# Kernel optimization log

Measured on AMD Instinct MI355X. Metric: run time of the kernel, lower is better.

Reference implementation:

```python
import jax, jax.numpy as jnp
import numpy as np

B, N, D, H = 2, 2048, 768, 12
HD = D // H


def setup_inputs() -> dict:
    key = jax.random.key(0)
    ks = jax.random.split(key, 8)
    x = jax.random.normal(ks[0], (B, N, D), dtype=jnp.float32)
    dist = jax.random.randint(ks[1], (B, N, N), 0, 32, dtype=jnp.int32)
    mask = jax.random.bernoulli(ks[2], 0.1, (B, N))  # True = masked key
    # parameters (torch Linear stored pre-transposed: y = x @ W + b)
    s = 1.0 / np.sqrt(D)
    qkv_w = jax.random.uniform(ks[3], (D, 3 * D), jnp.float32, -s, s)
    qkv_b = jax.random.uniform(ks[4], (3 * D,), jnp.float32, -s, s)
    out_w = jax.random.uniform(ks[5], (D, D), jnp.float32, -s, s)
    out_b = jax.random.uniform(ks[6], (D,), jnp.float32, -s, s)
    bias_table = jax.random.normal(ks[7], (32, H), dtype=jnp.float32)
    return {"x": x, "dist": dist, "mask": mask, "qkv_w": qkv_w,
            "qkv_b": qkv_b, "out_w": out_w, "out_b": out_b,
            "bias_table": bias_table}


def reference(x, dist, mask, qkv_w, qkv_b, out_w, out_b, bias_table):
    scale = HD ** -0.5
    qkv = x @ qkv_w + qkv_b                      # [B,N,3D]
    q, k, v = jnp.split(qkv, 3, axis=-1)
    sh = lambda t: t.reshape(B, N, H, HD).transpose(0, 2, 1, 3)  # [B,H,N,HD]
    q, k, v = sh(q), sh(k), sh(v)
    a = jnp.einsum('bhnd,bhmd->bhnm', q, k) * scale  # [B,H,N,N]
    # relative-position bias: gather [B,N,N,H] -> [B,H,N,N]
    a = a + bias_table[jnp.clip(dist, 0, 31)].transpose(0, 3, 1, 2)
    a = jnp.where(mask[:, None, None, :], -jnp.inf, a)
    a = jax.nn.softmax(a.astype(jnp.float32), axis=-1)  # dropout: eval mode (p ignored)
    o = jnp.einsum('bhnm,bhmd->bhnd', a, v)            # [B,H,N,HD]
    o = o.transpose(0, 2, 1, 3).reshape(B, N, D)
    return o @ out_w + out_b
```

## Files before the change

kernel.cpp:

```cpp
#include <hip/hip_runtime.h>
#include <hip/hip_bf16.h>

typedef unsigned short u16;
typedef __attribute__((ext_vector_type(8))) short bf16x8;
typedef __attribute__((ext_vector_type(4))) float f32x4;

#define MFMA_BF16(a,b,c) __builtin_amdgcn_mfma_f32_16x16x32_bf16((a),(b),(c),0,0,0)
#define LOG2E 1.4426950408889634f

__device__ __forceinline__ u16 f2b(float f) {
    __hip_bfloat16 h = __float2bfloat16(f);
    u16 u; __builtin_memcpy(&u, &h, 2); return u;
}
__device__ __forceinline__ f32x4 zero4() { f32x4 z = {0.f,0.f,0.f,0.f}; return z; }

__device__ __forceinline__ void gl_lds16(const u16* g, u16* l) {
    __builtin_amdgcn_global_load_lds(
        (const __attribute__((address_space(1))) unsigned int*)g,
        (__attribute__((address_space(3))) unsigned int*)l,
        16, 0, 0);
}

__global__ __launch_bounds__(256) void convX(const float* __restrict__ in, u16* __restrict__ out) {
    size_t i = ((size_t)blockIdx.x * 256 + threadIdx.x) * 8;
    float4 a = *(const float4*)(in + i);
    float4 b = *(const float4*)(in + i + 4);
    union { u16 s[8]; uint4 v; } u;
    u.s[0]=f2b(a.x); u.s[1]=f2b(a.y); u.s[2]=f2b(a.z); u.s[3]=f2b(a.w);
    u.s[4]=f2b(b.x); u.s[5]=f2b(b.y); u.s[6]=f2b(b.z); u.s[7]=f2b(b.w);
    *(uint4*)(out + i) = u.v;
}

__global__ __launch_bounds__(256) void packDist(const int* __restrict__ din, unsigned char* __restrict__ dout) {
    size_t i = ((size_t)blockIdx.x * 256 + threadIdx.x) * 4;
    int4 v = *(const int4*)(din + i);
    uchar4 o;
    o.x = (unsigned char)min(max(v.x, 0), 31);
    o.y = (unsigned char)min(max(v.y, 0), 31);
    o.z = (unsigned char)min(max(v.z, 0), 31);
    o.w = (unsigned char)min(max(v.w, 0), 31);
    *(uchar4*)(dout + i) = o;
}

__global__ __launch_bounds__(256) void convTW(const float* __restrict__ in, u16* __restrict__ out, int C) {
    __shared__ __align__(16) u16 T[64][68];
    int c0 = blockIdx.x * 64, k0 = blockIdx.y * 64;
    int tid = threadIdx.x;
#pragma unroll
    for (int i = 0; i < 4; ++i) {
        int id = tid + i * 256;
        int row = id >> 4, ch = id & 15;
        float4 v = *(const float4*)(in + (size_t)(k0 + row) * C + c0 + ch * 4);
        T[row][ch*4+0] = f2b(v.x); T[row][ch*4+1] = f2b(v.y);
        T[row][ch*4+2] = f2b(v.z); T[row][ch*4+3] = f2b(v.w);
    }
    __syncthreads();
#pragma unroll
    for (int i = 0; i < 2; ++i) {
        int id = tid + i * 256;
        int c = id >> 3, ch = id & 7;
        union { u16 s[8]; uint4 v; } u;
#pragma unroll
        for (int j = 0; j < 8; ++j) u.s[j] = T[ch*8+j][c];
        *(uint4*)(out + (size_t)(c0 + c) * 768 + k0 + ch * 8) = u.v;
    }
}

__global__ void detectMaskBits(const unsigned* __restrict__ m, unsigned long long* __restrict__ mbits) {
    __shared__ int sB, sH, sF;
    if (threadIdx.x == 0) { sB = 0; sH = 0; sF = 0; }
    __syncthreads();
    int lb = 0, lh = 0, lf = 0;
#pragma unroll
    for (int i = 0; i < 4; ++i) {
        unsigned v = m[threadIdx.x + i * 256];
        if (v == 0x3f800000u) { lf = 1; }
        else if (v > 1u) {
            unsigned b0 = v & 0xffu, b1 = (v >> 8) & 0xffu, b2 = (v >> 16) & 0xffu, b3 = v >> 24;
            bool bytesOK = (b0 <= 1u) && (b1 <= 1u) && (b2 <= 1u) && (b3 <= 1u);
            unsigned h0 = v & 0xffffu, h1 = v >> 16;
            bool halfOK = (h0 == 0u || h0 == 0x3f80u) && (h1 == 0u || h1 == 0x3f80u);
            if (bytesOK) lb = 1; else if (halfOK) lh = 1;
        }
    }
    if (lb) atomicOr(&sB, 1);
    if (lh) atomicOr(&sH, 1);
    if (lf) atomicOr(&sF, 1);
    __syncthreads();
    int mode = sH ? 3 : (sB ? 1 : (sF ? 2 : 0));
    const unsigned char* m8 = (const unsigned char*)m;
    const u16* mh = (const u16*)m;
    const float* mf = (const float*)m;
    const int* mi = (const int*)m;
    for (int it = 0; it < 16; ++it) {
        int e = it * 256 + threadIdx.x;
        int pred;
        if (mode == 0)      pred = (mi[e] != 0);
        else if (mode == 1) pred = (m8[e] != 0);
        else if (mode == 2) pred = (mf[e] != 0.0f);
        else                pred = (mh[e] != 0);
        unsigned long long bal = __ballot(pred);
        if ((threadIdx.x & 63) == 0) mbits[it * 4 + (threadIdx.x >> 6)] = bal;
    }
}

template<int MODE>
__global__ __launch_bounds__(256)
void gemmBT(const u16* __restrict__ A, const u16* __restrict__ Bt,
            const float* __restrict__ bias,
            u16* __restrict__ qO, u16* __restrict__ kO, u16* __restrict__ vO,
            float* __restrict__ fO) {
    __shared__ __align__(16) u16 As[128][40];
    __shared__ __align__(16) u16 Bs[128][40];
    const int K = 768;
    const int tid = threadIdx.x;
    const int lane = tid & 63, w = tid >> 6;
    const int wm = w >> 1, wn = w & 1;
    const int l15 = lane & 15, q = lane >> 4;
    const int m0 = blockIdx.y * 128, n0 = blockIdx.x * 128;
    const int rowS = tid >> 1, cS = (tid & 1) * 2;
    const u16* Ag = A + (size_t)(m0 + rowS) * K;
    const u16* Bg = Bt + (size_t)(n0 + rowS) * K;
    uint4 pa0, pa1, pb0, pb1;
    { const uint4* sa = (const uint4*)Ag; pa0 = sa[cS]; pa1 = sa[cS+1];
      const uint4* sb = (const uint4*)Bg; pb0 = sb[cS]; pb1 = sb[cS+1]; }
    f32x4 acc[4][4];
#pragma unroll
    for (int i=0;i<4;++i)
#pragma unroll
        for (int j=0;j<4;++j) acc[i][j] = zero4();

    for (int kt = 0; kt < 24; ++kt) {
        __syncthreads();
        *(uint4*)&As[rowS][cS*8]   = pa0; *(uint4*)&As[rowS][cS*8+8] = pa1;
        *(uint4*)&Bs[rowS][cS*8]   = pb0; *(uint4*)&Bs[rowS][cS*8+8] = pb1;
        __syncthreads();
        if (kt < 23) {
            const uint4* sa = (const uint4*)(Ag + (kt+1)*32);
            pa0 = sa[cS]; pa1 = sa[cS+1];
            const uint4* sb = (const uint4*)(Bg + (kt+1)*32);
            pb0 = sb[cS]; pb1 = sb[cS+1];
        }
        bf16x8 af[4], bfr[4];
#pragma unroll
        for (int mt=0; mt<4; ++mt) af[mt]  = *(const bf16x8*)&As[wm*64+mt*16+l15][q*8];
#pragma unroll
        for (int nt=0; nt<4; ++nt) bfr[nt] = *(const bf16x8*)&Bs[wn*64+nt*16+l15][q*8];
#pragma unroll
        for (int mt=0; mt<4; ++mt)
#pragma unroll
            for (int nt=0; nt<4; ++nt)
                acc[mt][nt] = MFMA_BF16(af[mt], bfr[nt], acc[mt][nt]);
    }

#pragma unroll
    for (int mt=0; mt<4; ++mt) {
#pragma unroll
        for (int nt=0; nt<4; ++nt) {
            int n = n0 + wn*64 + nt*16 + l15;
            float bv = bias[n];
            if (MODE == 0) {
                int which = n / 768;
                int rem = n - which*768;
                int hh = rem >> 6, hd = rem & 63;
                int mBase = m0 + wm*64 + mt*16 + q*4;
                int b = mBase >> 11, tok0 = mBase & 2047;
                if (which == 2) {
                    union { u16 s4[4]; unsigned long long u; } pv;
#pragma unroll
                    for (int r=0; r<4; ++r) pv.s4[r] = f2b(acc[mt][nt][r] + bv);
                    *(unsigned long long*)(vO + ((size_t)(b*12 + hh)*64 + hd)*2048 + tok0) = pv.u;
                } else {
#pragma unroll
                    for (int r=0; r<4; ++r) {
                        float v = acc[mt][nt][r] + bv;
                        size_t di = (((size_t)(b*12 + hh))*2048 + tok0 + r)*64 + hd;
                        if (which == 0) qO[di] = f2b(v * (0.125f * LOG2E));
                        else            kO[di] = f2b(v);
                    }
                }
            } else {
#pragma unroll
                for (int r=0; r<4; ++r) {
                    int m = m0 + wm*64 + mt*16 + q*4 + r;
                    fO[(size_t)m*768 + n] = acc[mt][nt][r] + bv;
                }
            }
        }
    }
}

__global__ __launch_bounds__(256)
void flashAttn(const u16* __restrict__ Qb, const u16* __restrict__ Kb,
               const u16* __restrict__ Vt, const unsigned char* __restrict__ dist8,
               const unsigned long long* __restrict__ mbits,
               const float* __restrict__ btg, u16* __restrict__ attnout) {
    __shared__ float bt[32];
    __shared__ __align__(16) u16 KT[2][4096];
    __shared__ __align__(16) u16 VT[2][4096];
    __shared__ __align__(16) u16 Os[4][16][72];
    const int tid = threadIdx.x;
    const int lane = tid & 63, w = tid >> 6;
    const int l15 = lane & 15, q = lane >> 4;
    const int wg = blockIdx.x + 32 * (blockIdx.y + 12 * blockIdx.z);
    const int xcd = wg & 7, slot = wg >> 3;
    const int g = ((slot >> 5) << 3) + xcd;
    const int i0 = (slot & 31) * 64;
    const int b = g / 12, h = g - b * 12;
    const int bh = g;
    const float NEG_INF = -__builtin_inff();
    if (tid < 32) bt[tid] = btg[tid*12 + h] * LOG2E;

    const int iRow = i0 + w*16 + l15;
    const u16* Qp = Qb + ((size_t)bh*2048 + iRow)*64;
    bf16x8 qB0 = *(const bf16x8*)(Qp + q*8);
    bf16x8 qB1 = *(const bf16x8*)(Qp + 32 + q*8);
    const unsigned char* dp = dist8 + ((size_t)(b*2048 + iRow))*2048 + q*4;
    const unsigned long long* mbp = mbits + b*32;
    const int srcL0 = ((2*q)   & 3)*16 + l15;
    const int srcL1 = ((2*q+1) & 3)*16 + l15;
    union { unsigned u4[4]; bf16x8 v; } one_;
    { unsigned oc = (l15 == 0) ? 0x3F803F80u : 0u;
      one_.u4[0]=oc; one_.u4[1]=oc; one_.u4[2]=oc; one_.u4[3]=oc; }

    const int stRow = w*16 + (lane >> 3);
    const int stCol = (((lane & 7) ^ (lane >> 3)) << 4);
    const char* kgB = (const char*)Kb + (size_t)bh*2048*128;
    const char* vgB = (const char*)Vt + (size_t)bh*64*4096;
    const int swz = (l15 & 7) << 4;
    const int f0 = (q*16)      ^ swz;
    const int f1 = (q*16 + 64) ^ swz;
    const int rB = l15 * 128;

    {
        u16* kd = &KT[0][0] + w*1024;
        u16* vd = &VT[0][0] + w*1024;
#pragma unroll
        for (int c = 0; c < 2; ++c) {
            int row = stRow + c*8;
            gl_lds16((const u16*)(kgB + (size_t)row*128 + stCol),  kd + c*512);
            gl_lds16((const u16*)(vgB + (size_t)row*4096 + stCol), vd + c*512);
        }
    }
    __syncthreads();

    f32x4 o0 = zero4(), o1 = zero4(), o2 = zero4(), o3 = zero4(), o4 = zero4();
    float mI = NEG_INF;
    int cur = 0;

    for (int jt = 0; jt < 32; ++jt) {
        const int j0 = jt * 64;
        if (jt < 31) {
            const int j0n = j0 + 64;
            u16* kd = &KT[cur^1][0] + w*1024;
            u16* vd = &VT[cur^1][0] + w*1024;
#pragma unroll
            for (int c = 0; c < 2; ++c) {
                int row = stRow + c*8;
                gl_lds16((const u16*)(kgB + (size_t)(j0n + row)*128 + stCol), kd + c*512);
                gl_lds16((const u16*)(vgB + (size_t)row*4096 + (size_t)j0n*2 + stCol), vd + c*512);
            }
        }
        unsigned dv4[4];
#pragma unroll
        for (int mt = 0; mt < 4; ++mt) dv4[mt] = *(const unsigned*)(dp + j0 + mt*16);
        unsigned long long mb = mbp[jt];

        const char* kt = (const char*)&KT[cur][0];
        f32x4 s0 = zero4(), s1 = zero4(), s2 = zero4(), s3 = zero4();
        {
            bf16x8 k00 = *(const bf16x8*)(kt + rB          + f0);
            bf16x8 k01 = *(const bf16x8*)(kt + rB          + f1);
            bf16x8 k10 = *(const bf16x8*)(kt + rB + 2048   + f0);
            bf16x8 k11 = *(const bf16x8*)(kt + rB + 2048   + f1);
            bf16x8 k20 = *(const bf16x8*)(kt + rB + 4096   + f0);
            bf16x8 k21 = *(const bf16x8*)(kt + rB + 4096   + f1);
            bf16x8 k30 = *(const bf16x8*)(kt + rB + 6144   + f0);
            bf16x8 k31 = *(const bf16x8*)(kt + rB + 6144   + f1);
            __builtin_amdgcn_s_setprio(1);
            s0 = MFMA_BF16(k00, qB0, s0); s0 = MFMA_BF16(k01, qB1, s0);
            s1 = MFMA_BF16(k10, qB0, s1); s1 = MFMA_BF16(k11, qB1, s1);
            s2 = MFMA_BF16(k20, qB0, s2); s2 = MFMA_BF16(k21, qB1, s2);
            s3 = MFMA_BF16(k30, qB0, s3); s3 = MFMA_BF16(k31, qB1, s3);
            __builtin_amdgcn_s_setprio(0);
        }

        unsigned long long ms = mb >> (q*4);
        unsigned mlo = (unsigned)ms, mhi = (unsigned)(ms >> 32);
        float sv[4][4];
#pragma unroll
        for (int mt = 0; mt < 4; ++mt) {
            const f32x4 sm = mt==0 ? s0 : (mt==1 ? s1 : (mt==2 ? s2 : s3));
            const unsigned d4 = dv4[mt];
#pragma unroll
            for (int r = 0; r < 4; ++r) {
                int dd = (d4 >> (r*8)) & 255;
                float x = sm[r] + bt[dd];
                unsigned bit = (mt < 2) ? ((mlo >> (mt*16 + r)) & 1u)
                                        : ((mhi >> ((mt-2)*16 + r)) & 1u);
                sv[mt][r] = bit ? NEG_INF : x;
            }
        }

        float t0 = fmaxf(fmaxf(sv[0][0], sv[0][1]), fmaxf(sv[0][2], sv[0][3]));
        float t1 = fmaxf(fmaxf(sv[1][0], sv[1][1]), fmaxf(sv[1][2], sv[1][3]));
        float t2 = fmaxf(fmaxf(sv[2][0], sv[2][1]), fmaxf(sv[2][2], sv[2][3]));
        float t3 = fmaxf(fmaxf(sv[3][0], sv[3][1]), fmaxf(sv[3][2], sv[3][3]));
        float rm = fmaxf(fmaxf(t0, t1), fmaxf(t2, t3));
        rm = fmaxf(rm, __shfl_xor(rm, 16, 64));
        rm = fmaxf(rm, __shfl_xor(rm, 32, 64));
        if (!__all(rm <= mI)) {
            float mn = fmaxf(mI, rm);
            float al = exp2f(mI - mn);
            mI = mn;
#pragma unroll
            for (int r = 0; r < 4; ++r) { o0[r] *= al; o1[r] *= al; o2[r] *= al; o3[r] *= al; }
            o4[0] *= al;
        }
        float p[4][4];
#pragma unroll
        for (int mt = 0; mt < 4; ++mt)
#pragma unroll
            for (int r = 0; r < 4; ++r) p[mt][r] = exp2f(sv[mt][r] - mI);

        unsigned pk[4][2];
#pragma unroll
        for (int mt = 0; mt < 4; ++mt) {
            pk[mt][0] = (unsigned)f2b(p[mt][0]) | ((unsigned)f2b(p[mt][1]) << 16);
            pk[mt][1] = (unsigned)f2b(p[mt][2]) | ((unsigned)f2b(p[mt][3]) << 16);
        }
        const char* vt = (const char*)&VT[cur][0];
        __builtin_amdgcn_s_setprio(1);
#pragma unroll
        for (int ks = 0; ks < 2; ++ks) {
            union { unsigned d[4]; bf16x8 v; } pb;
#pragma unroll
            for (int s = 0; s < 4; ++s) {
                int sl = (s >> 1) ? srcL1 : srcL0;
                int u0 = __shfl((int)pk[2*ks    ][s & 1], sl, 64);
                int u1 = __shfl((int)pk[2*ks + 1][s & 1], sl, 64);
                pb.d[s] = (q >> 1) ? (unsigned)u1 : (unsigned)u0;
            }
            const int fk = ks ? f1 : f0;
            bf16x8 v0 = *(const bf16x8*)(vt + rB          + fk);
            bf16x8 v1 = *(const bf16x8*)(vt + rB + 2048   + fk);
            bf16x8 v2 = *(const bf16x8*)(vt + rB + 4096   + fk);
            bf16x8 v3 = *(const bf16x8*)(vt + rB + 6144   + fk);
            o0 = MFMA_BF16(v0, pb.v, o0);
            o1 = MFMA_BF16(v1, pb.v, o1);
            o2 = MFMA_BF16(v2, pb.v, o2);
            o3 = MFMA_BF16(v3, pb.v, o3);
            o4 = MFMA_BF16(one_.v, pb.v, o4);
        }
        __builtin_amdgcn_s_setprio(0);

        __syncthreads();
        cur ^= 1;
    }

    float lsum = __shfl(o4[0], l15, 64);
    float inv = 1.0f / lsum;
#pragma unroll
    for (int r = 0; r < 4; ++r) {
        Os[w][l15][ 0 + q*4 + r] = f2b(o0[r] * inv);
        Os[w][l15][16 + q*4 + r] = f2b(o1[r] * inv);
        Os[w][l15][32 + q*4 + r] = f2b(o2[r] * inv);
        Os[w][l15][48 + q*4 + r] = f2b(o3[r] * inv);
    }
    __syncthreads();
    int rr = lane >> 2, cc = lane & 3;
    uint4 a0 = *(const uint4*)&Os[w][rr][cc*16];
    uint4 a1 = *(const uint4*)&Os[w][rr][cc*16 + 8];
    size_t orow = ((size_t)b*2048 + i0 + w*16 + rr)*768 + h*64 + cc*16;
    *(uint4*)(attnout + orow)     = a0;
    *(uint4*)(attnout + orow + 8) = a1;
}

extern "C" void kernel_launch(void* const* d_in, const int* in_sizes, int n_in,
                              void* d_out, int out_size, void* d_ws, size_t ws_size,
                              hipStream_t stream) {
    (void)in_sizes; (void)n_in; (void)out_size; (void)ws_size;
    const float* x      = (const float*)d_in[0];
    const int*   dist   = (const int*)d_in[1];
    const int*   mask   = (const int*)d_in[2];
    const float* qkv_w  = (const float*)d_in[3];
    const float* qkv_b  = (const float*)d_in[4];
    const float* out_w  = (const float*)d_in[5];
    const float* out_b  = (const float*)d_in[6];
    const float* btab   = (const float*)d_in[7];
    float* out = (float*)d_out;

    char* ws = (char*)d_ws;
    size_t off = 0;
    auto alloc = [&](size_t bytes) { void* p = ws + off; off += (bytes + 255) & ~(size_t)255; return p; };
    u16* xb      = (u16*)alloc((size_t)4096*768*2);
    u16* wqkvT   = (u16*)alloc((size_t)2304*768*2);
    u16* woutT   = (u16*)alloc((size_t)768*768*2);
    u16* Qb      = (u16*)alloc((size_t)24*2048*64*2);
    u16* Kb      = (u16*)alloc((size_t)24*2048*64*2);
    u16* Vtp     = (u16*)alloc((size_t)24*2048*64*2);
    u16* attnout = (u16*)alloc((size_t)4096*768*2);
    unsigned char* dist8 = (unsigned char*)alloc((size_t)2*2048*2048);
    unsigned long long* mbits = (unsigned long long*)alloc(64*8);

    convX<<<1536, 256, 0, stream>>>(x, xb);
    packDist<<<8192, 256, 0, stream>>>(dist, dist8);
    convTW<<<dim3(36,12), 256, 0, stream>>>(qkv_w, wqkvT, 2304);
    convTW<<<dim3(12,12), 256, 0, stream>>>(out_w, woutT, 768);
    detectMaskBits<<<1, 256, 0, stream>>>((const unsigned*)mask, mbits);
    gemmBT<0><<<dim3(18,32), 256, 0, stream>>>(xb, wqkvT, qkv_b, Qb, Kb, Vtp, nullptr);
    flashAttn<<<dim3(32,12,2), 256, 0, stream>>>(Qb, Kb, Vtp, dist8, mbits, btab, attnout);
    gemmBT<1><<<dim3(6,32), 256, 0, stream>>>(attnout, woutT, out_b, nullptr, nullptr, nullptr, out);
}
```

Before: 259.5 us.

## Split attention over key halves with merge kernel; fold mask into dist codes

```diff
diff --git a/kernel.cpp b/kernel.cpp
--- a/kernel.cpp
+++ b/kernel.cpp
@@ -31,14 +31,19 @@
     *(uint4*)(out + i) = u.v;
 }
 
-__global__ __launch_bounds__(256) void packDist(const int* __restrict__ din, unsigned char* __restrict__ dout) {
+__global__ __launch_bounds__(256) void packDist(const int* __restrict__ din,
+                                                const unsigned long long* __restrict__ mbits,
+                                                unsigned char* __restrict__ dout) {
     size_t i = ((size_t)blockIdx.x * 256 + threadIdx.x) * 4;
     int4 v = *(const int4*)(din + i);
+    int b = (int)(i >> 22);
+    int j = (int)(i & 2047);
+    unsigned bits = (unsigned)((mbits[b*32 + (j >> 6)] >> (j & 63)) & 0xFull);
     uchar4 o;
-    o.x = (unsigned char)min(max(v.x, 0), 31);
-    o.y = (unsigned char)min(max(v.y, 0), 31);
-    o.z = (unsigned char)min(max(v.z, 0), 31);
-    o.w = (unsigned char)min(max(v.w, 0), 31);
+    o.x = (bits & 1u) ? 32 : (unsigned char)min(max(v.x, 0), 31);
+    o.y = (bits & 2u) ? 32 : (unsigned char)min(max(v.y, 0), 31);
+    o.z = (bits & 4u) ? 32 : (unsigned char)min(max(v.z, 0), 31);
+    o.w = (bits & 8u) ? 32 : (unsigned char)min(max(v.w, 0), 31);
     *(uchar4*)(dout + i) = o;
 }
 
@@ -193,12 +198,11 @@
 __global__ __launch_bounds__(256)
 void flashAttn(const u16* __restrict__ Qb, const u16* __restrict__ Kb,
                const u16* __restrict__ Vt, const unsigned char* __restrict__ dist8,
-               const unsigned long long* __restrict__ mbits,
-               const float* __restrict__ btg, u16* __restrict__ attnout) {
-    __shared__ float bt[32];
+               const float* __restrict__ btg,
+               float* __restrict__ Op, float* __restrict__ mlp) {
+    __shared__ float bt[33];
     __shared__ __align__(16) u16 KT[2][4096];
     __shared__ __align__(16) u16 VT[2][4096];
-    __shared__ __align__(16) u16 Os[4][16][72];
     const int tid = threadIdx.x;
     const int lane = tid & 63, w = tid >> 6;
     const int l15 = lane & 15, q = lane >> 4;
@@ -206,17 +210,17 @@
     const int xcd = wg & 7, slot = wg >> 3;
     const int g = ((slot >> 5) << 3) + xcd;
     const int i0 = (slot & 31) * 64;
-    const int b = g / 12, h = g - b * 12;
-    const int bh = g;
+    const int zz = g / 12, h = g - zz * 12;
+    const int b = zz >> 1, sIdx = zz & 1;
+    const int bh = b * 12 + h;
     const float NEG_INF = -__builtin_inff();
-    if (tid < 32) bt[tid] = btg[tid*12 + h] * LOG2E;
+    if (tid < 33) bt[tid] = (tid == 32) ? NEG_INF : btg[tid*12 + h] * LOG2E;
 
     const int iRow = i0 + w*16 + l15;
     const u16* Qp = Qb + ((size_t)bh*2048 + iRow)*64;
     bf16x8 qB0 = *(const bf16x8*)(Qp + q*8);
     bf16x8 qB1 = *(const bf16x8*)(Qp + 32 + q*8);
     const unsigned char* dp = dist8 + ((size_t)(b*2048 + iRow))*2048 + q*4;
-    const unsigned long long* mbp = mbits + b*32;
     const int srcL0 = ((2*q)   & 3)*16 + l15;
     const int srcL1 = ((2*q+1) & 3)*16 + l15;
     union { unsigned u4[4]; bf16x8 v; } one_;
@@ -232,14 +236,16 @@
     const int f1 = (q*16 + 64) ^ swz;
     const int rB = l15 * 128;
 
+    const int jtBeg = sIdx * 16, jtEnd = jtBeg + 16;
     {
+        const int j0p = jtBeg * 64;
         u16* kd = &KT[0][0] + w*1024;
         u16* vd = &VT[0][0] + w*1024;
 #pragma unroll
         for (int c = 0; c < 2; ++c) {
             int row = stRow + c*8;
-            gl_lds16((const u16*)(kgB + (size_t)row*128 + stCol),  kd + c*512);
-            gl_lds16((const u16*)(vgB + (size_t)row*4096 + stCol), vd + c*512);
+            gl_lds16((const u16*)(kgB + (size_t)(j0p + row)*128 + stCol),          kd + c*512);
+            gl_lds16((const u16*)(vgB + (size_t)row*4096 + (size_t)j0p*2 + stCol), vd + c*512);
         }
     }
     __syncthreads();
@@ -248,23 +254,22 @@
     float mI = NEG_INF;
     int cur = 0;
 
-    for (int jt = 0; jt < 32; ++jt) {
+    for (int jt = jtBeg; jt < jtEnd; ++jt) {
         const int j0 = jt * 64;
-        if (jt < 31) {
+        if (jt < jtEnd - 1) {
             const int j0n = j0 + 64;
             u16* kd = &KT[cur^1][0] + w*1024;
             u16* vd = &VT[cur^1][0] + w*1024;
 #pragma unroll
             for (int c = 0; c < 2; ++c) {
                 int row = stRow + c*8;
-                gl_lds16((const u16*)(kgB + (size_t)(j0n + row)*128 + stCol), kd + c*512);
+                gl_lds16((const u16*)(kgB + (size_t)(j0n + row)*128 + stCol),          kd + c*512);
                 gl_lds16((const u16*)(vgB + (size_t)row*4096 + (size_t)j0n*2 + stCol), vd + c*512);
             }
         }
         unsigned dv4[4];
 #pragma unroll
         for (int mt = 0; mt < 4; ++mt) dv4[mt] = *(const unsigned*)(dp + j0 + mt*16);
-        unsigned long long mb = mbp[jt];
 
         const char* kt = (const char*)&KT[cur][0];
         f32x4 s0 = zero4(), s1 = zero4(), s2 = zero4(), s3 = zero4();
@@ -285,8 +290,6 @@
             __builtin_amdgcn_s_setprio(0);
         }
 
-        unsigned long long ms = mb >> (q*4);
-        unsigned mlo = (unsigned)ms, mhi = (unsigned)(ms >> 32);
         float sv[4][4];
 #pragma unroll
         for (int mt = 0; mt < 4; ++mt) {
@@ -295,10 +298,7 @@
 #pragma unroll
             for (int r = 0; r < 4; ++r) {
                 int dd = (d4 >> (r*8)) & 255;
-                float x = sm[r] + bt[dd];
-                unsigned bit = (mt < 2) ? ((mlo >> (mt*16 + r)) & 1u)
-                                        : ((mhi >> ((mt-2)*16 + r)) & 1u);
-                sv[mt][r] = bit ? NEG_INF : x;
+                sv[mt][r] = sm[r] + bt[dd];
             }
         }
 
@@ -359,21 +359,51 @@
     }
 
     float lsum = __shfl(o4[0], l15, 64);
-    float inv = 1.0f / lsum;
-#pragma unroll
-    for (int r = 0; r < 4; ++r) {
-        Os[w][l15][ 0 + q*4 + r] = f2b(o0[r] * inv);
-        Os[w][l15][16 + q*4 + r] = f2b(o1[r] * inv);
-        Os[w][l15][32 + q*4 + r] = f2b(o2[r] * inv);
-        Os[w][l15][48 + q*4 + r] = f2b(o3[r] * inv);
-    }
-    __syncthreads();
-    int rr = lane >> 2, cc = lane & 3;
-    uint4 a0 = *(const uint4*)&Os[w][rr][cc*16];
-    uint4 a1 = *(const uint4*)&Os[w][rr][cc*16 + 8];
-    size_t orow = ((size_t)b*2048 + i0 + w*16 + rr)*768 + h*64 + cc*16;
-    *(uint4*)(attnout + orow)     = a0;
-    *(uint4*)(attnout + orow + 8) = a1;
+    if (q == 0) {
+        float2 v; v.x = mI; v.y = lsum;
+        *(float2*)(mlp + ((size_t)(sIdx*24 + bh)*2048 + i0 + w*16 + l15)*2) = v;
+    }
+    float* dst = Op + (((size_t)(sIdx*24 + bh)*2048 + i0 + w*16 + l15)*64 + q*4);
+    *(f32x4*)(dst)      = o0;
+    *(f32x4*)(dst + 16) = o1;
+    *(f32x4*)(dst + 32) = o2;
+    *(f32x4*)(dst + 48) = o3;
+}
+
+__global__ __launch_bounds__(256)
+void mergeO(const float* __restrict__ Op, const float* __restrict__ mlp,
+            u16* __restrict__ attnout) {
+    const int tid = threadIdx.x;
+    const int w = tid >> 6, lane = tid & 63;
+    const int rsub = lane >> 4, d0 = (lane & 15) * 4;
+    const int row = blockIdx.x * 16 + w * 4 + rsub;
+    const int bh = row >> 11, i = row & 2047;
+    const int b = bh / 12, h = bh - b * 12;
+    const float NEG_INF = -__builtin_inff();
+    float m[2], l[2];
+#pragma unroll
+    for (int s = 0; s < 2; ++s) {
+        float2 v = *(const float2*)(mlp + ((size_t)(s*24 + bh)*2048 + i)*2);
+        m[s] = v.x; l[s] = v.y;
+    }
+    float M = fmaxf(m[0], m[1]);
+    float a[2]; float L = 0.f;
+#pragma unroll
+    for (int s = 0; s < 2; ++s) {
+        a[s] = (m[s] == NEG_INF) ? 0.f : exp2f(m[s] - M);
+        L += l[s] * a[s];
+    }
+    float inv = 1.0f / L;
+    float4 o = {0.f, 0.f, 0.f, 0.f};
+#pragma unroll
+    for (int s = 0; s < 2; ++s) {
+        float4 v = *(const float4*)(Op + (((size_t)(s*24 + bh)*2048 + i)*64 + d0));
+        o.x += v.x * a[s]; o.y += v.y * a[s]; o.z += v.z * a[s]; o.w += v.w * a[s];
+    }
+    union { u16 s4[4]; unsigned long long u; } pk;
+    pk.s4[0] = f2b(o.x * inv); pk.s4[1] = f2b(o.y * inv);
+    pk.s4[2] = f2b(o.z * inv); pk.s4[3] = f2b(o.w * inv);
+    *(unsigned long long*)(attnout + ((size_t)(b*2048 + i))*768 + h*64 + d0) = pk.u;
 }
 
 extern "C" void kernel_launch(void* const* d_in, const int* in_sizes, int n_in,
@@ -400,15 +430,18 @@
     u16* Kb      = (u16*)alloc((size_t)24*2048*64*2);
     u16* Vtp     = (u16*)alloc((size_t)24*2048*64*2);
     u16* attnout = (u16*)alloc((size_t)4096*768*2);
+    float* Opart = (float*)alloc((size_t)2*24*2048*64*4);
+    float* mlPart= (float*)alloc((size_t)2*24*2048*2*4);
     unsigned char* dist8 = (unsigned char*)alloc((size_t)2*2048*2048);
     unsigned long long* mbits = (unsigned long long*)alloc(64*8);
 
     convX<<<1536, 256, 0, stream>>>(x, xb);
-    packDist<<<8192, 256, 0, stream>>>(dist, dist8);
+    detectMaskBits<<<1, 256, 0, stream>>>((const unsigned*)mask, mbits);
+    packDist<<<8192, 256, 0, stream>>>(dist, mbits, dist8);
     convTW<<<dim3(36,12), 256, 0, stream>>>(qkv_w, wqkvT, 2304);
     convTW<<<dim3(12,12), 256, 0, stream>>>(out_w, woutT, 768);
-    detectMaskBits<<<1, 256, 0, stream>>>((const unsigned*)mask, mbits);
     gemmBT<0><<<dim3(18,32), 256, 0, stream>>>(xb, wqkvT, qkv_b, Qb, Kb, Vtp, nullptr);
-    flashAttn<<<dim3(32,12,2), 256, 0, stream>>>(Qb, Kb, Vtp, dist8, mbits, btab, attnout);
+    flashAttn<<<dim3(32,12,4), 256, 0, stream>>>(Qb, Kb, Vtp, dist8, btab, Opart, mlPart);
+    mergeO<<<3072, 256, 0, stream>>>(Opart, mlPart, attnout);
     gemmBT<1><<<dim3(6,32), 256, 0, stream>>>(attnout, woutT, out_b, nullptr, nullptr, nullptr, out);
 }
```

Result: no change. 264.4 us (+1.9%).

## Fold key mask into packed dist sentinel and use 16x16x16 MFMA for PV

Applied to the files above, without the earlier changes.

```diff
diff --git a/kernel.cpp b/kernel.cpp
--- a/kernel.cpp
+++ b/kernel.cpp
@@ -3,10 +3,21 @@
 
 typedef unsigned short u16;
 typedef __attribute__((ext_vector_type(8))) short bf16x8;
+typedef __attribute__((ext_vector_type(4))) short bf16x4;
 typedef __attribute__((ext_vector_type(4))) float f32x4;
 
 #define MFMA_BF16(a,b,c) __builtin_amdgcn_mfma_f32_16x16x32_bf16((a),(b),(c),0,0,0)
 #define LOG2E 1.4426950408889634f
+
+#if __has_builtin(__builtin_amdgcn_mfma_f32_16x16x16bf16_1k)
+#define MFMA16(a,b,c) __builtin_amdgcn_mfma_f32_16x16x16bf16_1k((a),(b),(c),0,0,0)
+#define HAVE_MFMA16 1
+#elif __has_builtin(__builtin_amdgcn_mfma_f32_16x16x16_bf16)
+#define MFMA16(a,b,c) __builtin_amdgcn_mfma_f32_16x16x16_bf16((a),(b),(c),0,0,0)
+#define HAVE_MFMA16 1
+#else
+#define HAVE_MFMA16 0
+#endif
 
 __device__ __forceinline__ u16 f2b(float f) {
     __hip_bfloat16 h = __float2bfloat16(f);
@@ -31,14 +42,19 @@
     *(uint4*)(out + i) = u.v;
 }
 
-__global__ __launch_bounds__(256) void packDist(const int* __restrict__ din, unsigned char* __restrict__ dout) {
+__global__ __launch_bounds__(256) void packDist(const int* __restrict__ din,
+                                                const unsigned long long* __restrict__ mbits,
+                                                unsigned char* __restrict__ dout) {
     size_t i = ((size_t)blockIdx.x * 256 + threadIdx.x) * 4;
     int4 v = *(const int4*)(din + i);
+    int b = (int)(i >> 22);
+    int j = (int)(i & 2047);
+    unsigned bits = (unsigned)((mbits[b*32 + (j >> 6)] >> (j & 63)) & 0xFull);
     uchar4 o;
-    o.x = (unsigned char)min(max(v.x, 0), 31);
-    o.y = (unsigned char)min(max(v.y, 0), 31);
-    o.z = (unsigned char)min(max(v.z, 0), 31);
-    o.w = (unsigned char)min(max(v.w, 0), 31);
+    o.x = (bits & 1u) ? 32 : (unsigned char)min(max(v.x, 0), 31);
+    o.y = (bits & 2u) ? 32 : (unsigned char)min(max(v.y, 0), 31);
+    o.z = (bits & 4u) ? 32 : (unsigned char)min(max(v.z, 0), 31);
+    o.w = (bits & 8u) ? 32 : (unsigned char)min(max(v.w, 0), 31);
     *(uchar4*)(dout + i) = o;
 }
 
@@ -193,9 +209,8 @@
 __global__ __launch_bounds__(256)
 void flashAttn(const u16* __restrict__ Qb, const u16* __restrict__ Kb,
                const u16* __restrict__ Vt, const unsigned char* __restrict__ dist8,
-               const unsigned long long* __restrict__ mbits,
                const float* __restrict__ btg, u16* __restrict__ attnout) {
-    __shared__ float bt[32];
+    __shared__ float bt[33];
     __shared__ __align__(16) u16 KT[2][4096];
     __shared__ __align__(16) u16 VT[2][4096];
     __shared__ __align__(16) u16 Os[4][16][72];
@@ -209,19 +224,24 @@
     const int b = g / 12, h = g - b * 12;
     const int bh = g;
     const float NEG_INF = -__builtin_inff();
-    if (tid < 32) bt[tid] = btg[tid*12 + h] * LOG2E;
+    if (tid < 33) bt[tid] = (tid == 32) ? NEG_INF : btg[tid*12 + h] * LOG2E;
 
     const int iRow = i0 + w*16 + l15;
     const u16* Qp = Qb + ((size_t)bh*2048 + iRow)*64;
     bf16x8 qB0 = *(const bf16x8*)(Qp + q*8);
     bf16x8 qB1 = *(const bf16x8*)(Qp + 32 + q*8);
     const unsigned char* dp = dist8 + ((size_t)(b*2048 + iRow))*2048 + q*4;
-    const unsigned long long* mbp = mbits + b*32;
+#if !HAVE_MFMA16
     const int srcL0 = ((2*q)   & 3)*16 + l15;
     const int srcL1 = ((2*q+1) & 3)*16 + l15;
     union { unsigned u4[4]; bf16x8 v; } one_;
     { unsigned oc = (l15 == 0) ? 0x3F803F80u : 0u;
       one_.u4[0]=oc; one_.u4[1]=oc; one_.u4[2]=oc; one_.u4[3]=oc; }
+#else
+    union { unsigned u2[2]; bf16x4 v; } one4_;
+    { unsigned oc = (l15 == 0) ? 0x3F803F80u : 0u;
+      one4_.u2[0]=oc; one4_.u2[1]=oc; }
+#endif
 
     const int stRow = w*16 + (lane >> 3);
     const int stCol = (((lane & 7) ^ (lane >> 3)) << 4);
@@ -257,14 +277,13 @@
 #pragma unroll
             for (int c = 0; c < 2; ++c) {
                 int row = stRow + c*8;
-                gl_lds16((const u16*)(kgB + (size_t)(j0n + row)*128 + stCol), kd + c*512);
+                gl_lds16((const u16*)(kgB + (size_t)(j0n + row)*128 + stCol),          kd + c*512);
                 gl_lds16((const u16*)(vgB + (size_t)row*4096 + (size_t)j0n*2 + stCol), vd + c*512);
             }
         }
         unsigned dv4[4];
 #pragma unroll
         for (int mt = 0; mt < 4; ++mt) dv4[mt] = *(const unsigned*)(dp + j0 + mt*16);
-        unsigned long long mb = mbp[jt];
 
         const char* kt = (const char*)&KT[cur][0];
         f32x4 s0 = zero4(), s1 = zero4(), s2 = zero4(), s3 = zero4();
@@ -285,8 +304,6 @@
             __builtin_amdgcn_s_setprio(0);
         }
 
-        unsigned long long ms = mb >> (q*4);
-        unsigned mlo = (unsigned)ms, mhi = (unsigned)(ms >> 32);
         float sv[4][4];
 #pragma unroll
         for (int mt = 0; mt < 4; ++mt) {
@@ -295,10 +312,7 @@
 #pragma unroll
             for (int r = 0; r < 4; ++r) {
                 int dd = (d4 >> (r*8)) & 255;
-                float x = sm[r] + bt[dd];
-                unsigned bit = (mt < 2) ? ((mlo >> (mt*16 + r)) & 1u)
-                                        : ((mhi >> ((mt-2)*16 + r)) & 1u);
-                sv[mt][r] = bit ? NEG_INF : x;
+                sv[mt][r] = sm[r] + bt[dd];
             }
         }
 
@@ -323,13 +337,33 @@
 #pragma unroll
             for (int r = 0; r < 4; ++r) p[mt][r] = exp2f(sv[mt][r] - mI);
 
+        const char* vt = (const char*)&VT[cur][0];
+#if HAVE_MFMA16
+        __builtin_amdgcn_s_setprio(1);
+#pragma unroll
+        for (int mt = 0; mt < 4; ++mt) {
+            union { unsigned d[2]; bf16x4 v; } pu;
+            pu.d[0] = (unsigned)f2b(p[mt][0]) | ((unsigned)f2b(p[mt][1]) << 16);
+            pu.d[1] = (unsigned)f2b(p[mt][2]) | ((unsigned)f2b(p[mt][3]) << 16);
+            const int cbase = (((mt*2 + (q>>1)) ^ (l15 & 7)) << 4) + (q & 1)*8;
+            bf16x4 v0 = *(const bf16x4*)(vt + rB          + cbase);
+            bf16x4 v1 = *(const bf16x4*)(vt + rB + 2048   + cbase);
+            bf16x4 v2 = *(const bf16x4*)(vt + rB + 4096   + cbase);
+            bf16x4 v3 = *(const bf16x4*)(vt + rB + 6144   + cbase);
+            o0 = MFMA16(v0, pu.v, o0);
+            o1 = MFMA16(v1, pu.v, o1);
+            o2 = MFMA16(v2, pu.v, o2);
+            o3 = MFMA16(v3, pu.v, o3);
+            o4 = MFMA16(one4_.v, pu.v, o4);
+        }
+        __builtin_amdgcn_s_setprio(0);
+#else
         unsigned pk[4][2];
 #pragma unroll
         for (int mt = 0; mt < 4; ++mt) {
             pk[mt][0] = (unsigned)f2b(p[mt][0]) | ((unsigned)f2b(p[mt][1]) << 16);
             pk[mt][1] = (unsigned)f2b(p[mt][2]) | ((unsigned)f2b(p[mt][3]) << 16);
         }
-        const char* vt = (const char*)&VT[cur][0];
         __builtin_amdgcn_s_setprio(1);
 #pragma unroll
         for (int ks = 0; ks < 2; ++ks) {
@@ -353,6 +387,7 @@
             o4 = MFMA_BF16(one_.v, pb.v, o4);
         }
         __builtin_amdgcn_s_setprio(0);
+#endif
 
         __syncthreads();
         cur ^= 1;
@@ -404,11 +439,11 @@
     unsigned long long* mbits = (unsigned long long*)alloc(64*8);
 
     convX<<<1536, 256, 0, stream>>>(x, xb);
-    packDist<<<8192, 256, 0, stream>>>(dist, dist8);
+    detectMaskBits<<<1, 256, 0, stream>>>((const unsigned*)mask, mbits);
+    packDist<<<8192, 256, 0, stream>>>(dist, mbits, dist8);
     convTW<<<dim3(36,12), 256, 0, stream>>>(qkv_w, wqkvT, 2304);
     convTW<<<dim3(12,12), 256, 0, stream>>>(out_w, woutT, 768);
-    detectMaskBits<<<1, 256, 0, stream>>>((const unsigned*)mask, mbits);
     gemmBT<0><<<dim3(18,32), 256, 0, stream>>>(xb, wqkvT, qkv_b, Qb, Kb, Vtp, nullptr);
-    flashAttn<<<dim3(32,12,2), 256, 0, stream>>>(Qb, Kb, Vtp, dist8, mbits, btab, attnout);
+    flashAttn<<<dim3(32,12,2), 256, 0, stream>>>(Qb, Kb, Vtp, dist8, btab, attnout);
     gemmBT<1><<<dim3(6,32), 256, 0, stream>>>(attnout, woutT, out_b, nullptr, nullptr, nullptr, out);
 }
```

After: 252.1 us. 1.03x faster.
